# Optimization experiments

Measured on AMD Instinct MI355X. Metric: run time of the kernel, lower is better.

Reference implementation:

```python
import jax, jax.numpy as jnp
from jax import lax
import numpy as np

SQRT2 = float(np.sqrt(2.0))


def _linear(x, W, b):
    # torch Linear convention: W is (out, in)
    return x @ W.T + b


def _causal_cnn_glu(x, w, b):
    # x: (B, T, C). Causal pad k-1=4 on time, Conv1d C->2C k=5, GLU, residual.
    xp = jnp.pad(x, ((0, 0), (4, 0), (0, 0)))
    y = lax.conv_general_dilated(
        xp.transpose(0, 2, 1), w, window_strides=(1,), padding='VALID',
        dimension_numbers=('NCH', 'OIH', 'NCH'))
    y = y + b[None, :, None]
    y = y.transpose(0, 2, 1)  # (B, T, 2C)
    a, g = jnp.split(y, 2, axis=-1)
    return (a * jax.nn.sigmoid(g) + x) / SQRT2


def setup_inputs() -> dict:
    key = jax.random.key(0)
    ks = jax.random.split(key, 12)
    B, T_enc, T_dec, D, IN = 32, 1024, 2048, 256, 80
    s_d = 1.0 / np.sqrt(D)
    s_in = 1.0 / np.sqrt(IN)
    return {
        'encoder_outputs': jax.random.normal(ks[0], (B, T_enc, D), jnp.float32),
        'first_embedding': jax.random.normal(ks[1], (B, T_enc, D), jnp.float32),
        'mel_inputs': jax.random.uniform(ks[2], (B, T_dec, IN), jnp.float32),
        'W_lin': jax.random.normal(ks[3], (D, IN), jnp.float32) * s_in,
        'b_lin': jnp.zeros((D,), jnp.float32),
        'conv_w0': jax.random.normal(ks[4], (2 * D, D, 5), jnp.float32) * s_d,
        'conv_b0': jnp.zeros((2 * D,), jnp.float32),
        'conv_w1': jax.random.normal(ks[5], (2 * D, D, 5), jnp.float32) * s_d,
        'conv_b1': jnp.zeros((2 * D,), jnp.float32),
        'W_attn': jax.random.normal(ks[6], (D, D), jnp.float32) * s_d,
        'b_attn': jnp.zeros((D,), jnp.float32),
        'W_proj': jax.random.normal(ks[7], (IN, D), jnp.float32) * s_d,
        'b_proj': jnp.zeros((IN,), jnp.float32),
    }


def reference(encoder_outputs, first_embedding, mel_inputs,
              W_lin, b_lin, conv_w0, conv_b0, conv_w1, conv_b1,
              W_attn, b_attn, W_proj, b_proj):
    B, T_dec, _ = mel_inputs.shape
    D = encoder_outputs.shape[-1]
    x = _linear(mel_inputs, W_lin, b_lin)                    # (B, T_dec, 256)
    # prepend zero initial input, drop last frame (shift right)
    x = jnp.concatenate([jnp.zeros((B, 1, D), x.dtype), x], axis=1)[:, :-1, :]
    h = _causal_cnn_glu(x, conv_w0, conv_b0)                 # CNN layer 0
    q = _linear(h, W_attn, b_attn)                           # attention after layer 0
    scores = jnp.einsum('btd,bsd->bts', q, encoder_outputs)  # (B, T_dec, T_enc)
    attn = jax.nn.softmax(scores, axis=-1)
    c = jnp.einsum('bts,bsd->btd', attn, encoder_outputs + first_embedding)
    h = h + c
    h = _causal_cnn_glu(h, conv_w1, conv_b1)                 # CNN layer 1 (no attention)
    return _linear(h, W_proj, b_proj)                        # (B, T_dec, in_dim)
```

## Files before the change

kernel.cpp:

```cpp
#include <hip/hip_runtime.h>
#include <math.h>

#define BB 32
#define TD 2048
#define TE 1024
#define DIM 256
#define INDIM 80

typedef __attribute__((ext_vector_type(8))) _Float16 f16x8;
typedef __attribute__((ext_vector_type(4))) float f32x4;

__device__ __forceinline__ float sigmoidf_(float x){ return 1.f/(1.f+__expf(-x)); }

__device__ __forceinline__ void cp16(const _Float16* g, _Float16* l){
  __builtin_amdgcn_global_load_lds(
      (const __attribute__((address_space(1))) unsigned int*)g,
      (__attribute__((address_space(3))) unsigned int*)l, 16, 0, 0);
}

__global__ __launch_bounds__(256) void k_wprep(const float* __restrict__ w,
    _Float16* __restrict__ Wf)
{
  int i = blockIdx.x*256 + threadIdx.x;
  int o = i / 1280;
  int kk = i - o*1280;
  int tap = kk >> 8, ic = kk & 255;
  Wf[i] = (_Float16)w[(size_t)o*1280 + ic*5 + tap];
}

__global__ __launch_bounds__(256) void k_qwprep(const float* __restrict__ W,
    _Float16* __restrict__ Wh, _Float16* __restrict__ Wl)
{
  int i = blockIdx.x*256 + threadIdx.x;
  float f = W[i];
  _Float16 h = (_Float16)f;
  Wh[i] = h;
  Wl[i] = (_Float16)(f - (float)h);
}

__global__ __launch_bounds__(256) void k_lwprep(const float* __restrict__ W,
    _Float16* __restrict__ Wh, _Float16* __restrict__ Wl)
{
  int i = blockIdx.x*256 + threadIdx.x;
  int d = i / 96, k = i - d*96;
  float f = (k < INDIM) ? W[d*INDIM + k] : 0.f;
  _Float16 h = (_Float16)f;
  Wh[i] = h;
  Wl[i] = (_Float16)(f - (float)h);
}

__global__ __launch_bounds__(256) void k_pwprep(const float* __restrict__ W,
    _Float16* __restrict__ Wh, _Float16* __restrict__ Wl)
{
  int i = blockIdx.x*256 + threadIdx.x;
  float f = W[i];
  _Float16 h = (_Float16)f;
  Wh[i] = h;
  Wl[i] = (_Float16)(f - (float)h);
}

__global__ __launch_bounds__(256) void k_eprep(const float* __restrict__ enc,
    const float* __restrict__ emb, _Float16* __restrict__ Eh,
    _Float16* __restrict__ EVt)
{
  __shared__ float ls[64][65];
  int blk = blockIdx.x;
  int dt = blk & 3, st = (blk>>2) & 15, b = blk >> 6;
  int s0 = st*64, d0 = dt*64;
  int tid = threadIdx.x;
  for (int k=0;k<16;k++){
    int idx = k*256 + tid;
    int r = idx >> 6, c = idx & 63;
    size_t gi = ((size_t)b*TE + s0 + r)*DIM + d0 + c;
    float e = enc[gi];
    ls[r][c] = e + emb[gi];
    Eh[gi] = (_Float16)e;
  }
  __syncthreads();
  for (int k=0;k<16;k++){
    int idx = k*256 + tid;
    int r = idx >> 6, c = idx & 63;
    EVt[((size_t)b*DIM + d0 + r)*TE + s0 + c] = (_Float16)ls[c][r];
  }
}

__global__ __launch_bounds__(256) void k_lin_mfma(const float* __restrict__ mel,
    const _Float16* __restrict__ Wh, const _Float16* __restrict__ Wl,
    const float* __restrict__ bias, _Float16* __restrict__ X)
{
  __shared__ __align__(16) _Float16 ms[64*104];
  int blk = blockIdx.x;
  int b = blk >> 5;
  int t0 = (blk & 31) << 6;
  int tid = threadIdx.x;

  for (int i = tid; i < 64*12; i += 256){
    int row = i / 12, cg = (i - row*12) * 8;
    int t = t0 + row - 1;
    f16x8 v = {};
    if (t >= 0 && cg < INDIM){
      const float4* p = (const float4*)(mel + ((size_t)b*TD + t)*INDIM + cg);
      float4 f0 = p[0], f1 = p[1];
      v[0]=(_Float16)f0.x; v[1]=(_Float16)f0.y; v[2]=(_Float16)f0.z; v[3]=(_Float16)f0.w;
      v[4]=(_Float16)f1.x; v[5]=(_Float16)f1.y; v[6]=(_Float16)f1.z; v[7]=(_Float16)f1.w;
    }
    *(f16x8*)&ms[row*104 + cg] = v;
  }
  __syncthreads();

  int wave = tid >> 6, lane = tid & 63;
  int l15 = lane & 15, l4 = lane >> 4;
  int mb = wave << 4;

  f16x8 am[3];
  #pragma unroll
  for (int kc=0;kc<3;kc++) am[kc] = *(f16x8*)&ms[(mb + l15)*104 + kc*32 + l4*8];

  for (int dt=0; dt<16; dt++){
    size_t wrow = (size_t)(dt*16 + l15)*96 + l4*8;
    f32x4 a = (f32x4){0.f,0.f,0.f,0.f};
    #pragma unroll
    for (int kc=0;kc<3;kc++){
      f16x8 bh = *(const f16x8*)(Wh + wrow + kc*32);
      f16x8 bl = *(const f16x8*)(Wl + wrow + kc*32);
      a = __builtin_amdgcn_mfma_f32_16x16x32_f16(am[kc], bh, a, 0,0,0);
      a = __builtin_amdgcn_mfma_f32_16x16x32_f16(am[kc], bl, a, 0,0,0);
    }
    int d = dt*16 + l15;
    float bv = bias[d];
    #pragma unroll
    for (int r=0;r<4;r++){
      int m = mb + l4*4 + r;
      int t = t0 + m;
      X[((size_t)b*TD + t)*DIM + d] = (t==0) ? (_Float16)0.f : (_Float16)(a[r] + bv);
    }
  }
}

template<int TIN_F32, int TOUT_F32>
__global__ __launch_bounds__(256) void k_conv_mfma(const void* __restrict__ Xin_,
    const _Float16* __restrict__ Wf, const float* __restrict__ bias,
    void* __restrict__ Hout_)
{
  __shared__ __align__(16) _Float16 as[68*264];
  int id = blockIdx.x;
  int dtile = id & 3, mtile = id >> 2;
  int b = mtile >> 5;
  int t0 = (mtile & 31) << 6;
  int d0 = dtile << 6;
  int tid = threadIdx.x;

  for (int i = tid; i < 68*32; i += 256){
    int row = i >> 5, cg = (i & 31) << 3;
    int t = t0 - 4 + row;
    f16x8 v = {};
    if (t >= 0){
      if (TIN_F32){
        const float4* p = (const float4*)((const float*)Xin_ + ((size_t)b*TD + t)*DIM + cg);
        float4 f0 = p[0], f1 = p[1];
        v[0]=(_Float16)f0.x; v[1]=(_Float16)f0.y; v[2]=(_Float16)f0.z; v[3]=(_Float16)f0.w;
        v[4]=(_Float16)f1.x; v[5]=(_Float16)f1.y; v[6]=(_Float16)f1.z; v[7]=(_Float16)f1.w;
      } else {
        v = *(const f16x8*)((const _Float16*)Xin_ + ((size_t)b*TD + t)*DIM + cg);
      }
    }
    *(f16x8*)&as[row*264 + cg] = v;
  }
  __syncthreads();

  int lane = tid & 63, wave = tid >> 6;
  int l15 = lane & 15, l4 = lane >> 4;
  int dA = d0 + (wave << 4) + l15;

  const _Float16* pA = Wf + (size_t)dA*1280 + l4*8;
  const _Float16* pG = Wf + (size_t)(256 + dA)*1280 + l4*8;

  f32x4 aca[4], acg[4];
  #pragma unroll
  for (int mt=0;mt<4;mt++){ aca[mt]=(f32x4){0.f,0.f,0.f,0.f}; acg[mt]=(f32x4){0.f,0.f,0.f,0.f}; }

  f16x8 bA = *(const f16x8*)pA;
  f16x8 bG = *(const f16x8*)pG;
  #pragma unroll
  for (int kc = 0; kc < 40; ++kc){
    f16x8 nA = bA, nG = bG;
    if (kc < 39){
      nA = *(const f16x8*)(pA + (kc+1)*32);
      nG = *(const f16x8*)(pG + (kc+1)*32);
    }
    int tap = kc >> 3;
    int ic0 = (kc & 7) << 5;
    int abase = (l15 + tap)*264 + ic0 + l4*8;
    #pragma unroll
    for (int mt=0;mt<4;mt++){
      f16x8 av = *(f16x8*)&as[abase + mt*16*264];
      aca[mt] = __builtin_amdgcn_mfma_f32_16x16x32_f16(av, bA, aca[mt], 0,0,0);
      acg[mt] = __builtin_amdgcn_mfma_f32_16x16x32_f16(av, bG, acg[mt], 0,0,0);
    }
    bA = nA; bG = nG;
  }

  const float is2 = 0.7071067811865476f;
  float ba = bias[dA], bg = bias[256 + dA];
  #pragma unroll
  for (int mt=0; mt<4; mt++){
    #pragma unroll
    for (int r=0;r<4;r++){
      int m = mt*16 + l4*4 + r;
      size_t orow = ((size_t)b*TD + t0 + m)*DIM;
      float xr = TIN_F32 ? ((const float*)Xin_)[orow + dA]
                         : (float)as[(m+4)*264 + dA];
      float a = aca[mt][r] + ba;
      float g = acg[mt][r] + bg;
      float o = (a*sigmoidf_(g) + xr)*is2;
      if (TOUT_F32) ((float*)Hout_)[orow + dA] = o;
      else          ((_Float16*)Hout_)[orow + dA] = (_Float16)o;
    }
  }
}

__device__ __forceinline__ void stage_k(const _Float16* __restrict__ Ehb,
    _Float16* __restrict__ dst, int srow0, int wave, int lane)
{
  int r2 = lane >> 5, cu = lane & 31;
  #pragma unroll
  for (int ii=0; ii<8; ii++){
    int row = (ii*4 + wave)*2 + r2;
    cp16(Ehb + (size_t)(srow0 + row)*DIM + ((cu ^ (row & 7)) << 3),
         dst + (ii*4 + wave)*512);
  }
}

__global__ __launch_bounds__(256) void k_attn(float* __restrict__ H,
    const _Float16* __restrict__ Wqh, const _Float16* __restrict__ Wql,
    const float* __restrict__ bq,
    const _Float16* __restrict__ Eh, const _Float16* __restrict__ EVt)
{
  __shared__ __align__(16) _Float16 Kb[2][64*256];
  __shared__ __align__(16) _Float16 pb[64][72];
  __shared__ float alphas[64];
  __shared__ float linvs[64];

  int i = blockIdx.x;
  int b = (i & 7) | ((i >> 8) << 3);
  int t0 = ((i >> 3) & 31) << 6;
  int tid = threadIdx.x;
  int wave = tid >> 6, lane = tid & 63;
  int l15 = lane & 15, l4 = lane >> 4;
  int mb = wave << 4;

  const _Float16* Ehb = Eh + (size_t)b*TE*DIM;
  const _Float16* EVb = EVt + (size_t)b*DIM*TE;

  stage_k(Ehb, &Kb[0][0], 0, wave, lane);

  f16x8 ah[8];
  {
    const float* hrow = H + ((size_t)b*TD + t0 + mb + l15)*DIM;
    #pragma unroll
    for (int kc=0;kc<8;kc++){
      const float4* p = (const float4*)(hrow + kc*32 + l4*8);
      float4 f0 = p[0], f1 = p[1];
      f16x8 v;
      v[0]=(_Float16)f0.x; v[1]=(_Float16)f0.y; v[2]=(_Float16)f0.z; v[3]=(_Float16)f0.w;
      v[4]=(_Float16)f1.x; v[5]=(_Float16)f1.y; v[6]=(_Float16)f1.z; v[7]=(_Float16)f1.w;
      ah[kc] = v;
    }
  }

  f32x4 qacc[16];
  for (int ot=0;ot<16;ot++){
    size_t wrow = (size_t)(ot*16 + l15)*256 + l4*8;
    f32x4 a = (f32x4){0.f,0.f,0.f,0.f};
    #pragma unroll
    for (int kc=0;kc<8;kc++){
      f16x8 bh = *(const f16x8*)(Wqh + wrow + kc*32);
      f16x8 bl = *(const f16x8*)(Wql + wrow + kc*32);
      a = __builtin_amdgcn_mfma_f32_16x16x32_f16(ah[kc], bh, a, 0,0,0);
      a = __builtin_amdgcn_mfma_f32_16x16x32_f16(ah[kc], bl, a, 0,0,0);
    }
    qacc[ot] = a;
  }
  #pragma unroll
  for (int ot=0;ot<16;ot++){
    float bqv = bq[ot*16 + l15];
    #pragma unroll
    for (int r=0;r<4;r++) qacc[ot][r] += bqv;
  }

  #pragma unroll
  for (int ot=0;ot<16;ot++){
    int o = ot*16 + l15;
    #pragma unroll
    for (int r=0;r<4;r++)
      Kb[1][(mb + l4*4 + r)*256 + o] = (_Float16)qacc[ot][r];
  }
  __syncthreads();
  f16x8 aqh[8];
  #pragma unroll
  for (int kc=0;kc<8;kc++) aqh[kc] = *(f16x8*)&Kb[1][(mb + l15)*256 + kc*32 + l4*8];
  __syncthreads();
  #pragma unroll
  for (int ot=0;ot<16;ot++){
    int o = ot*16 + l15;
    #pragma unroll
    for (int r=0;r<4;r++){
      float v = qacc[ot][r];
      _Float16 h = (_Float16)v;
      Kb[1][(mb + l4*4 + r)*256 + o] = (_Float16)(v - (float)h);
    }
  }
  __syncthreads();
  f16x8 aql[8];
  #pragma unroll
  for (int kc=0;kc<8;kc++) aql[kc] = *(f16x8*)&Kb[1][(mb + l15)*256 + kc*32 + l4*8];
  __syncthreads();

  f32x4 oacc[4][4];
  #pragma unroll
  for (int mt=0;mt<4;mt++)
    #pragma unroll
    for (int dt=0;dt<4;dt++) oacc[mt][dt] = (f32x4){0.f,0.f,0.f,0.f};
  float mrun[4], lrun[4];
  #pragma unroll
  for (int r=0;r<4;r++){ mrun[r] = -3.0e38f; lrun[r] = 0.f; }
  int dq = wave << 6;
  int sw = l15 & 7;

  #pragma unroll 2
  for (int c = 0; c < 16; ++c){
    int cur = c & 1;
    int s0 = c << 6;
    if (c < 15) stage_k(Ehb, &Kb[cur^1][0], s0 + 64, wave, lane);

    f32x4 sacc[4];
    #pragma unroll
    for (int st=0;st<4;st++){
      const _Float16* kb = &Kb[cur][(st*16 + l15)*256];
      f32x4 a = (f32x4){0.f,0.f,0.f,0.f};
      #pragma unroll
      for (int kc=0;kc<8;kc++){
        f16x8 bh = *(const f16x8*)(kb + (((kc*4 + l4) ^ sw) << 3));
        a = __builtin_amdgcn_mfma_f32_16x16x32_f16(aqh[kc], bh, a, 0,0,0);
        a = __builtin_amdgcn_mfma_f32_16x16x32_f16(aql[kc], bh, a, 0,0,0);
      }
      sacc[st] = a;
    }

    f16x8 vv[2][4];
    #pragma unroll
    for (int kp=0;kp<2;kp++)
      #pragma unroll
      for (int dt=0;dt<4;dt++)
        vv[kp][dt] = *(const f16x8*)(EVb + (size_t)(dq + dt*16 + l15)*TE + s0 + kp*32 + l4*8);

    float alpha[4];
    #pragma unroll
    for (int r=0;r<4;r++){
      float cm = fmaxf(fmaxf(sacc[0][r], sacc[1][r]), fmaxf(sacc[2][r], sacc[3][r]));
      cm = fmaxf(cm, __shfl_xor(cm, 1));
      cm = fmaxf(cm, __shfl_xor(cm, 2));
      cm = fmaxf(cm, __shfl_xor(cm, 4));
      cm = fmaxf(cm, __shfl_xor(cm, 8));
      float mnew = fmaxf(mrun[r], cm);
      alpha[r] = __expf(mrun[r] - mnew);
      mrun[r] = mnew;
      float ps = 0.f;
      #pragma unroll
      for (int st=0;st<4;st++){
        float p = __expf(sacc[st][r] - mnew);
        sacc[st][r] = p;
        ps += p;
      }
      ps += __shfl_xor(ps, 1);
      ps += __shfl_xor(ps, 2);
      ps += __shfl_xor(ps, 4);
      ps += __shfl_xor(ps, 8);
      lrun[r] = lrun[r]*alpha[r] + ps;
    }

    #pragma unroll
    for (int st=0;st<4;st++)
      #pragma unroll
      for (int r=0;r<4;r++)
        pb[mb + l4*4 + r][st*16 + l15] = (_Float16)sacc[st][r];
    if (l15 == 0){
      #pragma unroll
      for (int r=0;r<4;r++) alphas[mb + l4*4 + r] = alpha[r];
    }
    asm volatile("s_waitcnt lgkmcnt(0)" ::: "memory");
    __builtin_amdgcn_s_barrier();

    #pragma unroll
    for (int mt=0;mt<4;mt++){
      #pragma unroll
      for (int r=0;r<4;r++){
        float av = alphas[mt*16 + l4*4 + r];
        #pragma unroll
        for (int dt=0;dt<4;dt++) oacc[mt][dt][r] *= av;
      }
    }
    #pragma unroll
    for (int kp=0;kp<2;kp++){
      f16x8 pa[4];
      #pragma unroll
      for (int mt=0;mt<4;mt++) pa[mt] = *(f16x8*)&pb[mt*16 + l15][kp*32 + l4*8];
      #pragma unroll
      for (int dt=0;dt<4;dt++){
        #pragma unroll
        for (int mt=0;mt<4;mt++)
          oacc[mt][dt] = __builtin_amdgcn_mfma_f32_16x16x32_f16(pa[mt], vv[kp][dt], oacc[mt][dt], 0,0,0);
      }
    }
    __syncthreads();
  }

  if (l15 == 0){
    #pragma unroll
    for (int r=0;r<4;r++) linvs[mb + l4*4 + r] = 1.f / lrun[r];
  }
  __syncthreads();
  #pragma unroll
  for (int mt=0;mt<4;mt++){
    #pragma unroll
    for (int r=0;r<4;r++){
      float li = linvs[mt*16 + l4*4 + r];
      int t = t0 + mt*16 + l4*4 + r;
      float* hp = &H[((size_t)b*TD + t)*DIM + dq];
      #pragma unroll
      for (int dt=0;dt<4;dt++)
        hp[dt*16 + l15] += oacc[mt][dt][r] * li;
    }
  }
}

__global__ __launch_bounds__(256) void k_proj_mfma(const _Float16* __restrict__ Hin,
    const _Float16* __restrict__ Wh, const _Float16* __restrict__ Wl,
    const float* __restrict__ bias, float* __restrict__ out)
{
  int blk = blockIdx.x;
  int b = blk >> 5;
  int t0 = (blk & 31) << 6;
  int tid = threadIdx.x;
  int wave = tid >> 6, lane = tid & 63;
  int l15 = lane & 15, l4 = lane >> 4;
  int mb = wave << 4;

  f16x8 ah[8];
  const _Float16* hrow = Hin + ((size_t)b*TD + t0 + mb + l15)*DIM;
  #pragma unroll
  for (int kc=0;kc<8;kc++) ah[kc] = *(const f16x8*)(hrow + kc*32 + l4*8);

  #pragma unroll
  for (int nt=0; nt<5; nt++){
    size_t wrow = (size_t)(nt*16 + l15)*256 + l4*8;
    f32x4 a = (f32x4){0.f,0.f,0.f,0.f};
    #pragma unroll
    for (int kc=0;kc<8;kc++){
      f16x8 bh = *(const f16x8*)(Wh + wrow + kc*32);
      f16x8 bl = *(const f16x8*)(Wl + wrow + kc*32);
      a = __builtin_amdgcn_mfma_f32_16x16x32_f16(ah[kc], bh, a, 0,0,0);
      a = __builtin_amdgcn_mfma_f32_16x16x32_f16(ah[kc], bl, a, 0,0,0);
    }
    int n = nt*16 + l15;
    float bv = bias[n];
    #pragma unroll
    for (int r=0;r<4;r++){
      int t = t0 + mb + l4*4 + r;
      out[((size_t)b*TD + t)*INDIM + n] = a[r] + bv;
    }
  }
}

extern "C" void kernel_launch(void* const* d_in, const int* in_sizes, int n_in,
                              void* d_out, int out_size, void* d_ws, size_t ws_size,
                              hipStream_t stream) {
  const float* enc   = (const float*)d_in[0];
  const float* emb   = (const float*)d_in[1];
  const float* mel   = (const float*)d_in[2];
  const float* W_lin = (const float*)d_in[3];
  const float* b_lin = (const float*)d_in[4];
  const float* w0    = (const float*)d_in[5];
  const float* b0    = (const float*)d_in[6];
  const float* w1    = (const float*)d_in[7];
  const float* b1    = (const float*)d_in[8];
  const float* Wq    = (const float*)d_in[9];
  const float* bq    = (const float*)d_in[10];
  const float* Wp    = (const float*)d_in[11];
  const float* bp    = (const float*)d_in[12];
  float* out = (float*)d_out;

  const size_t NTOK = (size_t)BB*TD*DIM;
  const size_t NE   = (size_t)BB*TE*DIM;
  _Float16* Xb  = (_Float16*)d_ws;
  float*    H   = (float*)(Xb + NTOK);
  _Float16* Wf0 = (_Float16*)(H + NTOK);
  _Float16* Wf1 = Wf0 + (size_t)512*1280;
  _Float16* Wqh = Wf1 + (size_t)512*1280;
  _Float16* Wql = Wqh + 65536;
  _Float16* Wlh = Wql + 65536;
  _Float16* Wll = Wlh + 24576;
  _Float16* Wph = Wll + 24576;
  _Float16* Wpl = Wph + 20480;
  _Float16* Eh  = Xb;
  _Float16* EVt = Xb + NE;
  _Float16* Pb  = Xb;

  k_wprep    <<<2560, 256, 0, stream>>>(w0, Wf0);
  k_wprep    <<<2560, 256, 0, stream>>>(w1, Wf1);
  k_qwprep   <<<256,  256, 0, stream>>>(Wq, Wqh, Wql);
  k_lwprep   <<<96,   256, 0, stream>>>(W_lin, Wlh, Wll);
  k_pwprep   <<<80,   256, 0, stream>>>(Wp, Wph, Wpl);
  k_lin_mfma <<<1024, 256, 0, stream>>>(mel, Wlh, Wll, b_lin, Xb);
  k_conv_mfma<0,1><<<4096, 256, 0, stream>>>(Xb, Wf0, b0, H);
  k_eprep    <<<2048, 256, 0, stream>>>(enc, emb, Eh, EVt);
  k_attn     <<<1024, 256, 0, stream>>>(H, Wqh, Wql, bq, Eh, EVt);
  k_conv_mfma<1,0><<<4096, 256, 0, stream>>>(H, Wf1, b1, Pb);
  k_proj_mfma<<<1024, 256, 0, stream>>>(Pb, Wph, Wpl, bp, out);
}
```

Measured before the change: 868.8 us.

## Halve attention key tile to 32 rows and defer softmax row-sum reduction

The attention kernel now streams keys in 32-row chunks instead of 64, which halves the K and P shared-memory buffers, presumably to let more blocks reside per CU. Q staging is swizzled and drops several barriers, and the cross-lane sum of softmax weights is deferred until after the loop. The kernel also skips the rescale of the output accumulators when every alpha equals one, and raises wave priority around the MFMA sections. The trade-off is twice as many loop iterations and barriers per block, with less work per barrier to hide latency.

```diff
diff --git a/kernel.cpp b/kernel.cpp
--- a/kernel.cpp
+++ b/kernel.cpp
@@ -219,12 +219,12 @@
   }
 }
 
-__device__ __forceinline__ void stage_k(const _Float16* __restrict__ Ehb,
+__device__ __forceinline__ void stage_k32(const _Float16* __restrict__ Ehb,
     _Float16* __restrict__ dst, int srow0, int wave, int lane)
 {
   int r2 = lane >> 5, cu = lane & 31;
   #pragma unroll
-  for (int ii=0; ii<8; ii++){
+  for (int ii=0; ii<4; ii++){
     int row = (ii*4 + wave)*2 + r2;
     cp16(Ehb + (size_t)(srow0 + row)*DIM + ((cu ^ (row & 7)) << 3),
          dst + (ii*4 + wave)*512);
@@ -236,8 +236,8 @@
     const float* __restrict__ bq,
     const _Float16* __restrict__ Eh, const _Float16* __restrict__ EVt)
 {
-  __shared__ __align__(16) _Float16 Kb[2][64*256];
-  __shared__ __align__(16) _Float16 pb[64][72];
+  __shared__ __align__(16) _Float16 Kb[2][32*256];
+  __shared__ __align__(16) _Float16 pb[64][40];
   __shared__ float alphas[64];
   __shared__ float linvs[64];
 
@@ -252,8 +252,6 @@
   const _Float16* Ehb = Eh + (size_t)b*TE*DIM;
   const _Float16* EVb = EVt + (size_t)b*DIM*TE;
 
-  stage_k(Ehb, &Kb[0][0], 0, wave, lane);
-
   f16x8 ah[8];
   {
     const float* hrow = H + ((size_t)b*TD + t0 + mb + l15)*DIM;
@@ -288,32 +286,41 @@
     for (int r=0;r<4;r++) qacc[ot][r] += bqv;
   }
 
+  _Float16* Kf = &Kb[0][0];
   #pragma unroll
   for (int ot=0;ot<16;ot++){
     int o = ot*16 + l15;
     #pragma unroll
-    for (int r=0;r<4;r++)
-      Kb[1][(mb + l4*4 + r)*256 + o] = (_Float16)qacc[ot][r];
-  }
-  __syncthreads();
+    for (int r=0;r<4;r++){
+      int row = mb + l4*4 + r;
+      Kf[row*256 + (o ^ ((row & 7) << 3))] = (_Float16)qacc[ot][r];
+    }
+  }
   f16x8 aqh[8];
-  #pragma unroll
-  for (int kc=0;kc<8;kc++) aqh[kc] = *(f16x8*)&Kb[1][(mb + l15)*256 + kc*32 + l4*8];
-  __syncthreads();
+  {
+    int row = mb + l15, sw8 = l15 & 7;
+    #pragma unroll
+    for (int kc=0;kc<8;kc++)
+      aqh[kc] = *(f16x8*)&Kf[row*256 + (((kc*4 + l4) ^ sw8) << 3)];
+  }
   #pragma unroll
   for (int ot=0;ot<16;ot++){
     int o = ot*16 + l15;
     #pragma unroll
     for (int r=0;r<4;r++){
+      int row = mb + l4*4 + r;
       float v = qacc[ot][r];
       _Float16 h = (_Float16)v;
-      Kb[1][(mb + l4*4 + r)*256 + o] = (_Float16)(v - (float)h);
-    }
-  }
-  __syncthreads();
+      Kf[row*256 + (o ^ ((row & 7) << 3))] = (_Float16)(v - (float)h);
+    }
+  }
   f16x8 aql[8];
-  #pragma unroll
-  for (int kc=0;kc<8;kc++) aql[kc] = *(f16x8*)&Kb[1][(mb + l15)*256 + kc*32 + l4*8];
+  {
+    int row = mb + l15, sw8 = l15 & 7;
+    #pragma unroll
+    for (int kc=0;kc<8;kc++)
+      aql[kc] = *(f16x8*)&Kf[row*256 + (((kc*4 + l4) ^ sw8) << 3)];
+  }
   __syncthreads();
 
   f32x4 oacc[4][4];
@@ -327,15 +334,25 @@
   int dq = wave << 6;
   int sw = l15 & 7;
 
+  stage_k32(Ehb, &Kb[0][0], 0, wave, lane);
+  asm volatile("s_waitcnt vmcnt(0)" ::: "memory");
+  __syncthreads();
+
   #pragma unroll 2
-  for (int c = 0; c < 16; ++c){
+  for (int c = 0; c < 32; ++c){
     int cur = c & 1;
-    int s0 = c << 6;
-    if (c < 15) stage_k(Ehb, &Kb[cur^1][0], s0 + 64, wave, lane);
-
-    f32x4 sacc[4];
-    #pragma unroll
-    for (int st=0;st<4;st++){
+    int s0 = c << 5;
+    if (c < 31) stage_k32(Ehb, &Kb[cur^1][0], s0 + 32, wave, lane);
+
+    f16x8 vv[4];
+    #pragma unroll
+    for (int dt=0;dt<4;dt++)
+      vv[dt] = *(const f16x8*)(EVb + (size_t)(dq + dt*16 + l15)*TE + s0 + l4*8);
+
+    f32x4 sacc[2];
+    __builtin_amdgcn_s_setprio(1);
+    #pragma unroll
+    for (int st=0;st<2;st++){
       const _Float16* kb = &Kb[cur][(st*16 + l15)*256];
       f32x4 a = (f32x4){0.f,0.f,0.f,0.f};
       #pragma unroll
@@ -346,18 +363,12 @@
       }
       sacc[st] = a;
     }
-
-    f16x8 vv[2][4];
-    #pragma unroll
-    for (int kp=0;kp<2;kp++)
-      #pragma unroll
-      for (int dt=0;dt<4;dt++)
-        vv[kp][dt] = *(const f16x8*)(EVb + (size_t)(dq + dt*16 + l15)*TE + s0 + kp*32 + l4*8);
+    __builtin_amdgcn_s_setprio(0);
 
     float alpha[4];
     #pragma unroll
     for (int r=0;r<4;r++){
-      float cm = fmaxf(fmaxf(sacc[0][r], sacc[1][r]), fmaxf(sacc[2][r], sacc[3][r]));
+      float cm = fmaxf(sacc[0][r], sacc[1][r]);
       cm = fmaxf(cm, __shfl_xor(cm, 1));
       cm = fmaxf(cm, __shfl_xor(cm, 2));
       cm = fmaxf(cm, __shfl_xor(cm, 4));
@@ -365,22 +376,14 @@
       float mnew = fmaxf(mrun[r], cm);
       alpha[r] = __expf(mrun[r] - mnew);
       mrun[r] = mnew;
-      float ps = 0.f;
-      #pragma unroll
-      for (int st=0;st<4;st++){
-        float p = __expf(sacc[st][r] - mnew);
-        sacc[st][r] = p;
-        ps += p;
-      }
-      ps += __shfl_xor(ps, 1);
-      ps += __shfl_xor(ps, 2);
-      ps += __shfl_xor(ps, 4);
-      ps += __shfl_xor(ps, 8);
-      lrun[r] = lrun[r]*alpha[r] + ps;
-    }
-
-    #pragma unroll
-    for (int st=0;st<4;st++)
+      float p0 = __expf(sacc[0][r] - mnew);
+      float p1 = __expf(sacc[1][r] - mnew);
+      sacc[0][r] = p0; sacc[1][r] = p1;
+      lrun[r] = lrun[r]*alpha[r] + (p0 + p1);
+    }
+
+    #pragma unroll
+    for (int st=0;st<2;st++)
       #pragma unroll
       for (int r=0;r<4;r++)
         pb[mb + l4*4 + r][st*16 + l15] = (_Float16)sacc[st][r];
@@ -391,30 +394,49 @@
     asm volatile("s_waitcnt lgkmcnt(0)" ::: "memory");
     __builtin_amdgcn_s_barrier();
 
-    #pragma unroll
-    for (int mt=0;mt<4;mt++){
+    float avs[4][4];
+    bool need = false;
+    #pragma unroll
+    for (int mt=0;mt<4;mt++)
       #pragma unroll
       for (int r=0;r<4;r++){
         float av = alphas[mt*16 + l4*4 + r];
+        avs[mt][r] = av;
+        need |= (av != 1.0f);
+      }
+    if (need){
+      #pragma unroll
+      for (int mt=0;mt<4;mt++)
         #pragma unroll
-        for (int dt=0;dt<4;dt++) oacc[mt][dt][r] *= av;
-      }
-    }
-    #pragma unroll
-    for (int kp=0;kp<2;kp++){
-      f16x8 pa[4];
-      #pragma unroll
-      for (int mt=0;mt<4;mt++) pa[mt] = *(f16x8*)&pb[mt*16 + l15][kp*32 + l4*8];
-      #pragma unroll
-      for (int dt=0;dt<4;dt++){
-        #pragma unroll
-        for (int mt=0;mt<4;mt++)
-          oacc[mt][dt] = __builtin_amdgcn_mfma_f32_16x16x32_f16(pa[mt], vv[kp][dt], oacc[mt][dt], 0,0,0);
-      }
-    }
+        for (int r=0;r<4;r++){
+          float av = avs[mt][r];
+          #pragma unroll
+          for (int dt=0;dt<4;dt++) oacc[mt][dt][r] *= av;
+        }
+    }
+    f16x8 pa[4];
+    #pragma unroll
+    for (int mt=0;mt<4;mt++) pa[mt] = *(f16x8*)&pb[mt*16 + l15][l4*8];
+    __builtin_amdgcn_s_setprio(1);
+    #pragma unroll
+    for (int dt=0;dt<4;dt++){
+      #pragma unroll
+      for (int mt=0;mt<4;mt++)
+        oacc[mt][dt] = __builtin_amdgcn_mfma_f32_16x16x32_f16(pa[mt], vv[dt], oacc[mt][dt], 0,0,0);
+    }
+    __builtin_amdgcn_s_setprio(0);
     __syncthreads();
   }
 
+  #pragma unroll
+  for (int r=0;r<4;r++){
+    float s = lrun[r];
+    s += __shfl_xor(s, 1);
+    s += __shfl_xor(s, 2);
+    s += __shfl_xor(s, 4);
+    s += __shfl_xor(s, 8);
+    lrun[r] = s;
+  }
   if (l15 == 0){
     #pragma unroll
     for (int r=0;r<4;r++) linvs[mb + l4*4 + r] = 1.f / lrun[r];
```

After: 920.9 us. 1.06x slower.
